# Performance work log

Hardware: AMD Instinct MI355X
Metric: run time of the kernel (lower is better)

The kernel has to match this reference:

```python
import jax, jax.numpy as jnp
import numpy as np


def setup_inputs() -> dict:
    key = jax.random.key(0)
    B, F, H, W, C_out = 8, 64, 128, 128, 32
    V = H * W                     # grid vertices
    E = 3 * V                     # edges; flattened connectivity has 6V entries -> degree 6
    F2 = F // 2
    dim_channel = 6 * F2          # 192
    mid = dim_channel // 2        # 96
    out_ch = 2 * C_out            # 64
    k1, k2, k3, k4 = jax.random.split(key, 4)
    features = jax.random.normal(k1, (B, F, E), dtype=jnp.float32)
    # each vertex appears exactly 6 times in the flattened connectivity
    conn_flat = jax.random.permutation(k2, jnp.tile(jnp.arange(V, dtype=jnp.int32), 6))
    connectivity = conn_flat.reshape(E, 2)
    W1 = jax.random.normal(k3, (dim_channel, mid), dtype=jnp.float32) / np.sqrt(dim_channel)
    b1 = jnp.zeros((mid,), dtype=jnp.float32)
    W2 = jax.random.normal(k4, (mid, out_ch), dtype=jnp.float32) / np.sqrt(mid)
    b2 = jnp.zeros((out_ch,), dtype=jnp.float32)
    return {"features": features, "connectivity": connectivity,
            "output_dim": (H, W, C_out), "W1": W1, "b1": b1, "W2": W2, "b2": b2}


def _occurrence_rank(edges):
    # occ[i] = number of j < i with edges[j] == edges[i] (matches the serial
    # images_index bookkeeping in the torch loop). Stable argsort groups equal
    # vertices while preserving original order within a group.
    n = edges.shape[0]
    order = jnp.argsort(edges)            # stable by default in jax
    sorted_e = edges[order]
    first = jnp.searchsorted(sorted_e, sorted_e, side='left')
    rank_sorted = (jnp.arange(n) - first).astype(jnp.int32)
    return jnp.zeros(n, dtype=jnp.int32).at[order].set(rank_sorted)


def reference(features, connectivity, output_dim, W1, b1, W2, b2):
    B, F, E = features.shape
    H, Wd, C_out = int(output_dim[0]), int(output_dim[1]), int(output_dim[2])
    V = H * Wd
    F2 = F // 2
    edges = connectivity.reshape(-1)                      # [2E]
    # [B, F, E] -> [B, E, F] -> [B, 2E, F/2]: one half-feature per edge endpoint
    mesh = jnp.transpose(features, (0, 2, 1)).reshape(B, 2 * E, F2)
    occ = _occurrence_rank(edges)                         # slot per endpoint, 0..5
    # scatter half-features into [B, V, 6, F/2]; (vertex, slot) pairs are unique
    img = jnp.zeros((B, V, 6, F2), features.dtype).at[:, edges, occ, :].set(mesh)
    x = img.reshape(B, H, Wd, 6 * F2).transpose(0, 3, 1, 2)   # [B, 6*F/2, H, W]
    # 1x1 ConvTranspose2d == pointwise GEMM (torch weight layout [in, out, 1, 1])
    y = jax.nn.relu(jnp.einsum('bihw,io->bohw', x, W1) + b1[None, :, None, None])
    out = jax.nn.relu(jnp.einsum('bihw,io->bohw', y, W2) + b2[None, :, None, None])
    return out
```

## Files before the change

### kernel.cpp

```cpp
#include <hip/hip_runtime.h>
#include <hip/hip_bf16.h>
#include <stdint.h>

namespace {
constexpr int Bb   = 8;
constexpr int Ff   = 64;
constexpr int Ee   = 49152;
constexpr int Vv   = 16384;
constexpr int F2   = 32;
constexpr int TWOE = 2 * Ee;
constexpr int MID  = 96;
constexpr int OUTC = 64;
}

typedef __attribute__((ext_vector_type(8))) short bf16x8;
typedef __attribute__((ext_vector_type(4))) float f32x4;

__global__ void zero_cnt(int* __restrict__ cnt) {
    int i = blockIdx.x * 256 + threadIdx.x;
    if (i < Vv) cnt[i] = 0;
}

__global__ void bucket_fill(const int* __restrict__ conn, int* __restrict__ cnt,
                            int* __restrict__ buckets) {
    int i = blockIdx.x * 256 + threadIdx.x;
    if (i >= TWOE) return;
    int v = conn[i];
    int pos = atomicAdd(&cnt[v], 1);
    if (pos < 6) buckets[v * 6 + pos] = i;
}

__global__ void sort6_inv(const int* __restrict__ buckets, int* __restrict__ dest) {
    int v = blockIdx.x * 256 + threadIdx.x;
    if (v >= Vv) return;
    int a[6];
#pragma unroll
    for (int k = 0; k < 6; ++k) a[k] = buckets[v * 6 + k];
#define CSWAP(x, y) { int lo = min(a[x], a[y]); int hi = max(a[x], a[y]); a[x] = lo; a[y] = hi; }
    CSWAP(1, 2) CSWAP(4, 5) CSWAP(0, 2) CSWAP(3, 5) CSWAP(0, 1) CSWAP(3, 4)
    CSWAP(2, 5) CSWAP(0, 3) CSWAP(1, 4) CSWAP(2, 4) CSWAP(1, 3) CSWAP(2, 3)
#undef CSWAP
#pragma unroll
    for (int k = 0; k < 6; ++k) dest[a[k]] = v * 6 + k;
}

__global__ void prep_weights(const float* __restrict__ W1, const float* __restrict__ W2,
                             __hip_bfloat16* __restrict__ w1f, __hip_bfloat16* __restrict__ w2f) {
    int tid = blockIdx.x * 256 + threadIdx.x;
    if (tid < 18432) {
        int j = tid & 7, l = (tid >> 3) & 63, ft = tid >> 9;
        int kk = ft / 6, nt = ft - kk * 6;
        int k = kk * 32 + (l >> 4) * 8 + j;
        int n = nt * 16 + (l & 15);
        w1f[tid] = __float2bfloat16(W1[k * MID + n]);
    } else if (tid < 24576) {
        int t2 = tid - 18432;
        int j = t2 & 7, l = (t2 >> 3) & 63, ft = t2 >> 9;
        int kk = ft >> 2, nt = ft & 3;
        int k = kk * 32 + (l >> 4) * 8 + j;
        int n = nt * 16 + (l & 15);
        w2f[t2] = __float2bfloat16(W2[k * OUTC + n]);
    }
}

__global__ __launch_bounds__(256) void scatter_feats(const float* __restrict__ feat,
                                                     const int* __restrict__ dest,
                                                     ushort* __restrict__ xg) {
    __shared__ float tile[64][65];
    const int b  = blockIdx.y;
    const int e0 = blockIdx.x * 64;
    const int t  = threadIdx.x;
    const float* src = feat + (size_t)b * Ff * Ee;
#pragma unroll
    for (int k = 0; k < 16; ++k) {
        int idx = k * 256 + t;
        int c = idx >> 6;
        int e = idx & 63;
        tile[c][e] = src[(size_t)c * Ee + e0 + e];
    }
    __syncthreads();
    ushort* dst_base = xg + (size_t)b * ((size_t)Vv * 192);
#pragma unroll
    for (int it = 0; it < 2; ++it) {
        int item = it * 256 + t;
        int le = item >> 2, s2 = item & 3;
        int e = le >> 1, h = le & 1;
        int i = e0 * 2 + e * 2 + h;
        int d = dest[i];
        int c0 = h * 32 + s2 * 8;
        union { ushort u[8]; uint4 q; } pk;
#pragma unroll
        for (int k = 0; k < 8; ++k) {
            __hip_bfloat16 hv = __float2bfloat16(tile[c0 + k][e]);
            pk.u[k] = *reinterpret_cast<ushort*>(&hv);
        }
        *reinterpret_cast<uint4*>(dst_base + (size_t)d * 32 + s2 * 8) = pk.q;
    }
}

__global__ __launch_bounds__(256) void decode_mfma(
    const ushort* __restrict__ xg,
    const __hip_bfloat16* __restrict__ w1f, const float* __restrict__ b1,
    const __hip_bfloat16* __restrict__ w2f, const float* __restrict__ b2,
    float* __restrict__ out)
{
    __shared__ __align__(16) __hip_bfloat16 ys[64][104];
    const int t   = threadIdx.x;
    const int l   = t & 63;
    const int wid = t >> 6;
    const int b   = blockIdx.y;
    const int v0  = blockIdx.x * 64 + wid * 16;
    const int lr  = l & 15;
    const int lg  = l >> 4;

    const ushort* xv = xg + ((size_t)b * Vv + v0) * 192;

    f32x4 acc[6];
#pragma unroll
    for (int nt = 0; nt < 6; ++nt) {
        float bv = b1[nt * 16 + lr];
        acc[nt] = (f32x4){bv, bv, bv, bv};
    }
#pragma unroll
    for (int kk = 0; kk < 6; ++kk) {
        bf16x8 a = *reinterpret_cast<const bf16x8*>(xv + (size_t)lr * 192 + kk * 32 + lg * 8);
#pragma unroll
        for (int nt = 0; nt < 6; ++nt) {
            bf16x8 w = *reinterpret_cast<const bf16x8*>(w1f + ((size_t)((kk * 6 + nt) * 64 + l) * 8));
            acc[nt] = __builtin_amdgcn_mfma_f32_16x16x32_bf16(a, w, acc[nt], 0, 0, 0);
        }
    }
#pragma unroll
    for (int nt = 0; nt < 6; ++nt) {
#pragma unroll
        for (int r = 0; r < 4; ++r) {
            ys[wid * 16 + lg * 4 + r][nt * 16 + lr] = __float2bfloat16(fmaxf(acc[nt][r], 0.0f));
        }
    }
    __syncthreads();

    f32x4 acc2[4];
#pragma unroll
    for (int nt = 0; nt < 4; ++nt) {
        float bv = b2[nt * 16 + lr];
        acc2[nt] = (f32x4){bv, bv, bv, bv};
    }
#pragma unroll
    for (int kk = 0; kk < 3; ++kk) {
        bf16x8 a = *reinterpret_cast<const bf16x8*>(&ys[wid * 16 + lr][kk * 32 + lg * 8]);
#pragma unroll
        for (int nt = 0; nt < 4; ++nt) {
            bf16x8 w = *reinterpret_cast<const bf16x8*>(w2f + ((size_t)((kk * 4 + nt) * 64 + l) * 8));
            acc2[nt] = __builtin_amdgcn_mfma_f32_16x16x32_bf16(a, w, acc2[nt], 0, 0, 0);
        }
    }

    const int vbase = v0 + lg * 4;
#pragma unroll
    for (int nt = 0; nt < 4; ++nt) {
        f32x4 o4;
#pragma unroll
        for (int r = 0; r < 4; ++r) o4[r] = fmaxf(acc2[nt][r], 0.0f);
        *reinterpret_cast<f32x4*>(out + (((size_t)(b * OUTC + nt * 16 + lr)) << 14) + vbase) = o4;
    }
}

extern "C" void kernel_launch(void* const* d_in, const int* in_sizes, int n_in,
                              void* d_out, int out_size, void* d_ws, size_t ws_size,
                              hipStream_t stream) {
    const float* feat = (const float*)d_in[0];
    const int*   conn = (const int*)d_in[1];
    const float* W1   = (const float*)d_in[3];
    const float* b1   = (const float*)d_in[4];
    const float* W2   = (const float*)d_in[5];
    const float* b2   = (const float*)d_in[6];
    float* out = (float*)d_out;

    char* ws = (char*)d_ws;
    int* cnt     = (int*)ws;
    int* buckets = (int*)(ws + 65536);
    int* dest    = (int*)(ws + 65536 + 393216);
    __hip_bfloat16* w1f = (__hip_bfloat16*)(ws + 65536 + 2 * 393216);
    __hip_bfloat16* w2f = w1f + 18432;
    ushort* xg = (ushort*)(ws + 65536 + 2 * 393216 + 49152);

    zero_cnt<<<(Vv + 255) / 256, 256, 0, stream>>>(cnt);
    bucket_fill<<<(TWOE + 255) / 256, 256, 0, stream>>>(conn, cnt, buckets);
    sort6_inv<<<(Vv + 255) / 256, 256, 0, stream>>>(buckets, dest);
    prep_weights<<<96, 256, 0, stream>>>(W1, W2, w1f, w2f);
    scatter_feats<<<dim3(Ee / 64, Bb), 256, 0, stream>>>(feat, dest, xg);
    decode_mfma<<<dim3(Vv / 64, Bb), 256, 0, stream>>>(xg, w1f, b1, w2f, b2, out);
}
```

Measured before the change: 67.50 us.

## Fuse all stages into one cooperative persistent kernel with grid syncs

Replaces six separate launches with a single cooperative kernel of 384 persistent blocks. Grid-wide syncs separate counter init and weight prep, bucket fill, the small sort, the feature scatter and the two-layer MFMA decode. The intermediate layout now interleaves batch pairs per vertex, so each MFMA A-row loads contiguous data for two batches and the feature tile is staged as bf16 in shared memory with vectorized float4 loads. This removes launch gaps and the per-kernel tail, but adds the cost of grid.sync and relies on cooperative launch support, with the old kernels kept as a fallback.

Result: slower. 258.0 us (+282.2%).

```diff
diff --git a/kernel.cpp b/kernel.cpp
--- a/kernel.cpp
+++ b/kernel.cpp
@@ -1,52 +1,188 @@
 #include <hip/hip_runtime.h>
 #include <hip/hip_bf16.h>
+#include <hip/hip_cooperative_groups.h>
 #include <stdint.h>
+
+namespace cg = cooperative_groups;
 
 namespace {
 constexpr int Bb   = 8;
 constexpr int Ff   = 64;
 constexpr int Ee   = 49152;
 constexpr int Vv   = 16384;
-constexpr int F2   = 32;
 constexpr int TWOE = 2 * Ee;
 constexpr int MID  = 96;
 constexpr int OUTC = 64;
+constexpr int NBLK = 384;
 }
 
 typedef __attribute__((ext_vector_type(8))) short bf16x8;
 typedef __attribute__((ext_vector_type(4))) float f32x4;
-
-__global__ void zero_cnt(int* __restrict__ cnt) {
-    int i = blockIdx.x * 256 + threadIdx.x;
-    if (i < Vv) cnt[i] = 0;
-}
-
-__global__ void bucket_fill(const int* __restrict__ conn, int* __restrict__ cnt,
-                            int* __restrict__ buckets) {
-    int i = blockIdx.x * 256 + threadIdx.x;
-    if (i >= TWOE) return;
-    int v = conn[i];
-    int pos = atomicAdd(&cnt[v], 1);
-    if (pos < 6) buckets[v * 6 + pos] = i;
-}
-
-__global__ void sort6_inv(const int* __restrict__ buckets, int* __restrict__ dest) {
-    int v = blockIdx.x * 256 + threadIdx.x;
-    if (v >= Vv) return;
-    int a[6];
-#pragma unroll
-    for (int k = 0; k < 6; ++k) a[k] = buckets[v * 6 + k];
+typedef __attribute__((ext_vector_type(2))) float f32x2;
+typedef __attribute__((ext_vector_type(4))) unsigned int u32x4;
+
+__global__ __launch_bounds__(256, 2) void fused_all(
+    const float* __restrict__ feat, const int* __restrict__ conn,
+    const float* __restrict__ W1, const float* __restrict__ b1,
+    const float* __restrict__ W2, const float* __restrict__ b2,
+    float* __restrict__ out, int* __restrict__ cnt, int* __restrict__ buckets,
+    int* __restrict__ dest, __hip_bfloat16* __restrict__ w1f,
+    __hip_bfloat16* __restrict__ w2f, ushort* __restrict__ xg)
+{
+    cg::grid_group grid = cg::this_grid();
+    __shared__ __align__(16) union {
+        ushort tile[2][64][72];
+        __hip_bfloat16 ys[64][104];
+    } sm;
+    const int t    = threadIdx.x;
+    const int bid  = blockIdx.x;
+    const int gtid = bid * 256 + t;
+
+    if (gtid < Vv) cnt[gtid] = 0;
+    if (gtid < 18432) {
+        int j = gtid & 7, l = (gtid >> 3) & 63, ft = gtid >> 9;
+        int kk = ft / 6, nt = ft - kk * 6;
+        int k = kk * 32 + (l >> 4) * 8 + j;
+        int n = nt * 16 + (l & 15);
+        w1f[gtid] = __float2bfloat16(W1[k * MID + n]);
+    } else if (gtid < 24576) {
+        int t2 = gtid - 18432;
+        int j = t2 & 7, l = (t2 >> 3) & 63, ft = t2 >> 9;
+        int kk = ft >> 2, nt = ft & 3;
+        int k = kk * 32 + (l >> 4) * 8 + j;
+        int n = nt * 16 + (l & 15);
+        w2f[t2] = __float2bfloat16(W2[k * OUTC + n]);
+    }
+    grid.sync();
+
+    {
+        int v = conn[gtid];
+        int pos = atomicAdd(&cnt[v], 1);
+        if (pos < 6) buckets[v * 6 + pos] = gtid;
+    }
+    grid.sync();
+
+    if (gtid < Vv) {
+        int a[6];
+#pragma unroll
+        for (int k = 0; k < 6; ++k) a[k] = buckets[gtid * 6 + k];
 #define CSWAP(x, y) { int lo = min(a[x], a[y]); int hi = max(a[x], a[y]); a[x] = lo; a[y] = hi; }
-    CSWAP(1, 2) CSWAP(4, 5) CSWAP(0, 2) CSWAP(3, 5) CSWAP(0, 1) CSWAP(3, 4)
-    CSWAP(2, 5) CSWAP(0, 3) CSWAP(1, 4) CSWAP(2, 4) CSWAP(1, 3) CSWAP(2, 3)
+        CSWAP(1, 2) CSWAP(4, 5) CSWAP(0, 2) CSWAP(3, 5) CSWAP(0, 1) CSWAP(3, 4)
+        CSWAP(2, 5) CSWAP(0, 3) CSWAP(1, 4) CSWAP(2, 4) CSWAP(1, 3) CSWAP(2, 3)
 #undef CSWAP
 #pragma unroll
-    for (int k = 0; k < 6; ++k) dest[a[k]] = v * 6 + k;
-}
-
-__global__ void prep_weights(const float* __restrict__ W1, const float* __restrict__ W2,
-                             __hip_bfloat16* __restrict__ w1f, __hip_bfloat16* __restrict__ w2f) {
+        for (int k = 0; k < 6; ++k) dest[a[k]] = gtid * 6 + k;
+    }
+    grid.sync();
+
+    {
+        const int c  = t >> 2;
+        const int l4 = t & 3;
+        for (int vb = bid; vb < 3072; vb += NBLK) {
+            const int e0 = (vb >> 2) * 64;
+            const int g  = vb & 3;
+#pragma unroll
+            for (int q = 0; q < 2; ++q) {
+                const float* src = feat + ((size_t)(2 * g + q) * Ff + c) * Ee + e0;
+#pragma unroll
+                for (int k = 0; k < 4; ++k) {
+                    int e = k * 16 + l4 * 4;
+                    float4 d = *reinterpret_cast<const float4*>(src + e);
+                    __hip_bfloat16 h0 = __float2bfloat16(d.x);
+                    __hip_bfloat16 h1 = __float2bfloat16(d.y);
+                    __hip_bfloat16 h2 = __float2bfloat16(d.z);
+                    __hip_bfloat16 h3 = __float2bfloat16(d.w);
+                    sm.tile[q][e + 0][c] = *reinterpret_cast<ushort*>(&h0);
+                    sm.tile[q][e + 1][c] = *reinterpret_cast<ushort*>(&h1);
+                    sm.tile[q][e + 2][c] = *reinterpret_cast<ushort*>(&h2);
+                    sm.tile[q][e + 3][c] = *reinterpret_cast<ushort*>(&h3);
+                }
+            }
+            __syncthreads();
+            const size_t base_g = (size_t)g * ((size_t)Vv * 384);
+#pragma unroll
+            for (int it = 0; it < 4; ++it) {
+                int task = it * 256 + t;
+                int ie = task >> 3;
+                int r  = task & 7;
+                int e  = ie >> 1, h = ie & 1;
+                int q  = r >> 2,  j = r & 3;
+                int d  = dest[e0 * 2 + ie];
+                u32x4 qv = *reinterpret_cast<const u32x4*>(&sm.tile[q][e][h * 32 + j * 8]);
+                *reinterpret_cast<u32x4*>(xg + base_g + (size_t)d * 64 + r * 8) = qv;
+            }
+            __syncthreads();
+        }
+    }
+    grid.sync();
+
+    {
+        const int l   = t & 63;
+        const int wid = t >> 6;
+        const int lr  = l & 15;
+        const int lg  = l >> 4;
+        for (int vb = bid; vb < 2048; vb += NBLK) {
+            const int g  = vb >> 9;
+            const int vw = (vb & 511) * 32 + wid * 8;
+            const ushort* xa = xg + (size_t)g * ((size_t)Vv * 384)
+                             + ((size_t)(vw + (lr >> 1)) * 6) * 64 + (lr & 1) * 32 + lg * 8;
+            f32x4 acc[6];
+#pragma unroll
+            for (int nt = 0; nt < 6; ++nt) {
+                float bv = b1[nt * 16 + lr];
+                acc[nt] = (f32x4){bv, bv, bv, bv};
+            }
+#pragma unroll
+            for (int kk = 0; kk < 6; ++kk) {
+                bf16x8 a = *reinterpret_cast<const bf16x8*>(xa + kk * 64);
+#pragma unroll
+                for (int nt = 0; nt < 6; ++nt) {
+                    bf16x8 w = *reinterpret_cast<const bf16x8*>(w1f + ((size_t)((kk * 6 + nt) * 64 + l) * 8));
+                    acc[nt] = __builtin_amdgcn_mfma_f32_16x16x32_bf16(a, w, acc[nt], 0, 0, 0);
+                }
+            }
+#pragma unroll
+            for (int nt = 0; nt < 6; ++nt) {
+#pragma unroll
+                for (int r = 0; r < 4; ++r) {
+                    sm.ys[wid * 16 + lg * 4 + r][nt * 16 + lr] = __float2bfloat16(fmaxf(acc[nt][r], 0.0f));
+                }
+            }
+            __syncthreads();
+            f32x4 acc2[4];
+#pragma unroll
+            for (int nt = 0; nt < 4; ++nt) {
+                float bv = b2[nt * 16 + lr];
+                acc2[nt] = (f32x4){bv, bv, bv, bv};
+            }
+#pragma unroll
+            for (int kk = 0; kk < 3; ++kk) {
+                bf16x8 a = *reinterpret_cast<const bf16x8*>(&sm.ys[wid * 16 + lr][kk * 32 + lg * 8]);
+#pragma unroll
+                for (int nt = 0; nt < 4; ++nt) {
+                    bf16x8 w = *reinterpret_cast<const bf16x8*>(w2f + ((size_t)((kk * 4 + nt) * 64 + l) * 8));
+                    acc2[nt] = __builtin_amdgcn_mfma_f32_16x16x32_bf16(a, w, acc2[nt], 0, 0, 0);
+                }
+            }
+#pragma unroll
+            for (int nt = 0; nt < 4; ++nt) {
+                int o = nt * 16 + lr;
+                f32x2 p0 = {fmaxf(acc2[nt][0], 0.0f), fmaxf(acc2[nt][2], 0.0f)};
+                f32x2 p1 = {fmaxf(acc2[nt][1], 0.0f), fmaxf(acc2[nt][3], 0.0f)};
+                int vv = vw + 2 * lg;
+                *reinterpret_cast<f32x2*>(out + ((size_t)((2 * g + 0) * OUTC + o) << 14) + vv) = p0;
+                *reinterpret_cast<f32x2*>(out + ((size_t)((2 * g + 1) * OUTC + o) << 14) + vv) = p1;
+            }
+            __syncthreads();
+        }
+    }
+}
+
+__global__ void prep_misc(const float* __restrict__ W1, const float* __restrict__ W2,
+                          __hip_bfloat16* __restrict__ w1f, __hip_bfloat16* __restrict__ w2f,
+                          int* __restrict__ cnt) {
     int tid = blockIdx.x * 256 + threadIdx.x;
+    if (tid < Vv) cnt[tid] = 0;
     if (tid < 18432) {
         int j = tid & 7, l = (tid >> 3) & 63, ft = tid >> 9;
         int kk = ft / 6, nt = ft - kk * 6;
@@ -63,9 +199,32 @@
     }
 }
 
-__global__ __launch_bounds__(256) void scatter_feats(const float* __restrict__ feat,
-                                                     const int* __restrict__ dest,
-                                                     ushort* __restrict__ xg) {
+__global__ void bucket_fill(const int* __restrict__ conn, int* __restrict__ cnt,
+                            int* __restrict__ buckets) {
+    int i = blockIdx.x * 256 + threadIdx.x;
+    if (i >= TWOE) return;
+    int v = conn[i];
+    int pos = atomicAdd(&cnt[v], 1);
+    if (pos < 6) buckets[v * 6 + pos] = i;
+}
+
+__global__ void sort6_inv(const int* __restrict__ buckets, int* __restrict__ dest) {
+    int v = blockIdx.x * 256 + threadIdx.x;
+    if (v >= Vv) return;
+    int a[6];
+#pragma unroll
+    for (int k = 0; k < 6; ++k) a[k] = buckets[v * 6 + k];
+#define CSWAP(x, y) { int lo = min(a[x], a[y]); int hi = max(a[x], a[y]); a[x] = lo; a[y] = hi; }
+    CSWAP(1, 2) CSWAP(4, 5) CSWAP(0, 2) CSWAP(3, 5) CSWAP(0, 1) CSWAP(3, 4)
+    CSWAP(2, 5) CSWAP(0, 3) CSWAP(1, 4) CSWAP(2, 4) CSWAP(1, 3) CSWAP(2, 3)
+#undef CSWAP
+#pragma unroll
+    for (int k = 0; k < 6; ++k) dest[a[k]] = v * 6 + k;
+}
+
+__global__ __launch_bounds__(256) void scatter_feats_fb(const float* __restrict__ feat,
+                                                        const int* __restrict__ dest,
+                                                        ushort* __restrict__ xg) {
     __shared__ float tile[64][65];
     const int b  = blockIdx.y;
     const int e0 = blockIdx.x * 64;
@@ -88,17 +247,17 @@
         int i = e0 * 2 + e * 2 + h;
         int d = dest[i];
         int c0 = h * 32 + s2 * 8;
-        union { ushort u[8]; uint4 q; } pk;
+        union { ushort u[8]; u32x4 qv; } pk;
 #pragma unroll
         for (int k = 0; k < 8; ++k) {
             __hip_bfloat16 hv = __float2bfloat16(tile[c0 + k][e]);
             pk.u[k] = *reinterpret_cast<ushort*>(&hv);
         }
-        *reinterpret_cast<uint4*>(dst_base + (size_t)d * 32 + s2 * 8) = pk.q;
-    }
-}
-
-__global__ __launch_bounds__(256) void decode_mfma(
+        *reinterpret_cast<u32x4*>(dst_base + (size_t)d * 32 + s2 * 8) = pk.qv;
+    }
+}
+
+__global__ __launch_bounds__(256) void decode_mfma_fb(
     const ushort* __restrict__ xg,
     const __hip_bfloat16* __restrict__ w1f, const float* __restrict__ b1,
     const __hip_bfloat16* __restrict__ w2f, const float* __restrict__ b2,
@@ -112,7 +271,6 @@
     const int v0  = blockIdx.x * 64 + wid * 16;
     const int lr  = l & 15;
     const int lg  = l >> 4;
-
     const ushort* xv = xg + ((size_t)b * Vv + v0) * 192;
 
     f32x4 acc[6];
@@ -138,7 +296,6 @@
         }
     }
     __syncthreads();
-
     f32x4 acc2[4];
 #pragma unroll
     for (int nt = 0; nt < 4; ++nt) {
@@ -154,7 +311,6 @@
             acc2[nt] = __builtin_amdgcn_mfma_f32_16x16x32_bf16(a, w, acc2[nt], 0, 0, 0);
         }
     }
-
     const int vbase = v0 + lg * 4;
 #pragma unroll
     for (int nt = 0; nt < 4; ++nt) {
@@ -184,10 +340,17 @@
     __hip_bfloat16* w2f = w1f + 18432;
     ushort* xg = (ushort*)(ws + 65536 + 2 * 393216 + 49152);
 
-    zero_cnt<<<(Vv + 255) / 256, 256, 0, stream>>>(cnt);
-    bucket_fill<<<(TWOE + 255) / 256, 256, 0, stream>>>(conn, cnt, buckets);
-    sort6_inv<<<(Vv + 255) / 256, 256, 0, stream>>>(buckets, dest);
-    prep_weights<<<96, 256, 0, stream>>>(W1, W2, w1f, w2f);
-    scatter_feats<<<dim3(Ee / 64, Bb), 256, 0, stream>>>(feat, dest, xg);
-    decode_mfma<<<dim3(Vv / 64, Bb), 256, 0, stream>>>(xg, w1f, b1, w2f, b2, out);
-}
+    void* args[] = { (void*)&feat, (void*)&conn, (void*)&W1, (void*)&b1,
+                     (void*)&W2,   (void*)&b2,   (void*)&out, (void*)&cnt,
+                     (void*)&buckets, (void*)&dest, (void*)&w1f, (void*)&w2f,
+                     (void*)&xg };
+    hipError_t err = hipLaunchCooperativeKernel((const void*)fused_all, dim3(NBLK),
+                                                dim3(256), args, 0, stream);
+    if (err != hipSuccess) {
+        prep_misc<<<96, 256, 0, stream>>>(W1, W2, w1f, w2f, cnt);
+        bucket_fill<<<(TWOE + 255) / 256, 256, 0, stream>>>(conn, cnt, buckets);
+        sort6_inv<<<(Vv + 255) / 256, 256, 0, stream>>>(buckets, dest);
+        scatter_feats_fb<<<dim3(Ee / 64, Bb), 256, 0, stream>>>(feat, dest, xg);
+        decode_mfma_fb<<<dim3(Vv / 64, Bb), 256, 0, stream>>>(xg, w1f, b1, w2f, b2, out);
+    }
+}
```
